# Performance work log

Hardware: AMD Instinct MI355X
Metric: run time of the kernel (lower is better)

The kernel has to match this reference:

```python
import jax, jax.numpy as jnp
import numpy as np

N, H, E, K = 256, 128, 64, 4  # nodes, hidden, dist-embed dim, heads
ALPHA = 0.2  # leaky-relu slope


def setup_inputs() -> dict:
    key = jax.random.key(0)
    ks = jax.random.split(key, 12)
    s = lambda k, sh: (jax.random.normal(k, sh, jnp.float32) * 0.05)
    return dict(
        action_hidden_state=jax.random.normal(ks[0], (N, H), jnp.float32),
        goal_hidden_state=jax.random.normal(ks[1], (N, H), jnp.float32),
        goal=jax.random.normal(ks[2], (N, 2), jnp.float32),
        action=jax.random.normal(ks[3], (N, 2), jnp.float32),
        W_emb=s(ks[4], (1, E)), b_emb=jnp.zeros((E,), jnp.float32),
        W_gate=s(ks[5], (2 * E + 2 * H, H)), b_gate=jnp.zeros((H,), jnp.float32),
        W_gat=s(ks[6], (K, H, H)), a_src=s(ks[7], (K, H)), a_dst=s(ks[8], (K, H)),
        gat_bias=jnp.zeros((H,), jnp.float32),
    )


def cal_dist(goal, action):
    # Vectorized, math-faithful (incl. source typos) version of the O(n^2) loop.
    ax, ay = action[:, 0], action[:, 1]
    gx, gy = goal[:, 0], goal[:, 1]
    a1x, a1y = ax[:, None], ay[:, None]   # node i
    a2x, a2y = ax[None, :], ay[None, :]   # node j
    g1x, g1y = gx[:, None], gy[:, None]
    g2x, g2y = gx[None, :], gy[None, :]
    dn = (a1x - a1x) * (g1y - g2y) - (a1y - a2y) * (g1x - g2x)
    cross_a = a1x * a2y - a1y * a2x
    gterm = g1x * g2y - g1x * g2x
    n1 = cross_a * (g1x - g2x) - (a1x - a2x) * gterm
    n2 = cross_a * (g1y - g2y) - (a1y - a2x) * gterm
    safe = jnp.where(dn == 0.0, 1.0, dn)
    p1, p2 = n1 / safe, n2 / safe
    base = jnp.linalg.norm(action - goal, axis=-1)  # [n]
    d1p = jnp.sqrt((a1x - p1) ** 2 + (a1y - p2) ** 2)
    d2p = jnp.sqrt((a2x - p1) ** 2 + (a2y - p2) ** 2)
    cond = (dn != 0.0) & ((a1x - p1) * (p1 - g1x) > 0.0)
    ones = jnp.ones_like(dn)
    d1 = jnp.where(cond, d1p, base[:, None] * ones)
    d2 = jnp.where(cond, d2p, base[None, :] * ones)
    n = d1.shape[0]
    ii = jnp.arange(n)[:, None]
    jj = jnp.arange(n)[None, :]
    # dist[i,j]=d1(i,j) for i<j; dist[j,i]=d2(i,j) i.e. lower triangle = d2.T; diag = |a_i - g_i|
    return jnp.where(ii == jj, base[:, None] * ones, jnp.where(ii < jj, d1, d2.T))


def reference(action_hidden_state, goal_hidden_state, goal, action,
              W_emb, b_emb, W_gate, b_gate, W_gat, a_src, a_dst, gat_bias):
    ha, hg = action_hidden_state, goal_hidden_state
    n, h = ha.shape
    dist = cal_dist(goal, action)                      # [n,n]
    emb = dist[..., None] * W_emb[0] + b_emb           # Linear(1,E) -> [n,n,E]
    # pairwise interaction gate (i != idx branch, computed for all pairs)
    gate_in = jnp.concatenate([
        jnp.broadcast_to(ha[:, None, :], (n, n, h)),
        jnp.broadcast_to(ha[None, :, :], (n, n, h)),
        emb, jnp.swapaxes(emb, 0, 1)], axis=-1)        # [n,n,2H+2E]
    gate = jax.nn.sigmoid(gate_in @ W_gate + b_gate)   # [n,n,H]
    gated = ha[None, :, :] * gate
    # self branch: gates the goal hidden state; action row stays ungated
    emb_d = emb[jnp.arange(n), jnp.arange(n)]          # [n,E]
    gate_self = jax.nn.sigmoid(
        jnp.concatenate([ha, hg, emb_d, emb_d], axis=-1) @ W_gate + b_gate)
    curr_goal = hg * gate_self                         # [n,H]
    eye = jnp.eye(n, dtype=bool)[..., None]
    curr_action = jnp.where(eye, ha[:, None, :], gated)          # [n,n,H]
    gat_in = jnp.concatenate([curr_action, curr_goal[:, None, :]], axis=1)  # [n,n+1,H]
    # multi-head GAT layer (batched over the n query nodes)
    hp = jnp.einsum('bmf,kfo->bkmo', gat_in, W_gat)    # [n,K,m,H]
    attn = (jnp.einsum('bkmo,ko->bkm', hp, a_src)[..., :, None]
            + jnp.einsum('bkmo,ko->bkm', hp, a_dst)[..., None, :])  # [n,K,m,m]
    attn = jax.nn.softmax(jax.nn.leaky_relu(attn, ALPHA), axis=-1)
    out = jnp.einsum('bkij,bkjo->bkio', attn, hp).mean(axis=1) + gat_bias  # [n,m,H]
    out = jax.nn.elu(out)
    idx = jnp.arange(n)
    return out[idx, idx]                               # [n,H]
```

## Files before the change

### kernel.cpp

```cpp
#include <hip/hip_runtime.h>
#include <math.h>

#define N 256
#define H 128
#define E 64
#define K 4
#define M (N + 1)
#define WAVES 16
#define BLOCK 1024

__device__ __forceinline__ float sigm(float x) {
    return __fdividef(1.0f, 1.0f + __expf(-x));
}

__device__ __forceinline__ float wave_sum(float v) {
#pragma unroll
    for (int d = 1; d < 64; d <<= 1) v += __shfl_xor(v, d, 64);
    return v;
}

__device__ __forceinline__ float readlane_f(float v, int l) {
    return __uint_as_float(__builtin_amdgcn_readlane(__float_as_uint(v), l));
}

__device__ __forceinline__ float kbutterfly(float q0, float q1, float q2, float q3,
                                            int lane) {
    const bool b1 = lane & 1;
    const bool b2 = lane & 2;
    float aA = b1 ? q1 : q0, aB = b1 ? q0 : q1;
    aA += __shfl_xor(aB, 1, 64);
    float cA = b1 ? q3 : q2, cB = b1 ? q2 : q3;
    cA += __shfl_xor(cB, 1, 64);
    float eA = b2 ? cA : aA, eB = b2 ? aA : cA;
    eA += __shfl_xor(eB, 2, 64);
#pragma unroll
    for (int d = 4; d < 64; d <<= 1) eA += __shfl_xor(eA, d, 64);
    return eA;
}

__device__ __forceinline__ void pairdist(
    float a1x, float a1y, float a2x, float a2y,
    float g1x, float g1y, float g2x, float g2y,
    float baseR, float baseC, float& d_rc, float& d_cr)
{
    float t  = __fmul_rn(__fsub_rn(a1y, a2y), __fsub_rn(g1x, g2x));
    float dn = -t;
    float ca = __fsub_rn(__fmul_rn(a1x, a2y), __fmul_rn(a1y, a2x));
    float gt = __fsub_rn(__fmul_rn(g1x, g2y), __fmul_rn(g1x, g2x));
    float n1 = __fsub_rn(__fmul_rn(ca, __fsub_rn(g1x, g2x)),
                         __fmul_rn(__fsub_rn(a1x, a2x), gt));
    float n2 = __fsub_rn(__fmul_rn(ca, __fsub_rn(g1y, g2y)),
                         __fmul_rn(__fsub_rn(a1y, a2x), gt));
    float safe = (dn == 0.0f) ? 1.0f : dn;
    float p1 = __fdiv_rn(n1, safe);
    float p2 = __fdiv_rn(n2, safe);
    bool cond = (dn != 0.0f) &&
                (__fmul_rn(__fsub_rn(a1x, p1), __fsub_rn(p1, g1x)) > 0.0f);
    float dx1 = __fsub_rn(a1x, p1), dy1 = __fsub_rn(a1y, p2);
    float d1p = __fsqrt_rn(__fadd_rn(__fmul_rn(dx1, dx1), __fmul_rn(dy1, dy1)));
    float dx2 = __fsub_rn(a2x, p1), dy2 = __fsub_rn(a2y, p2);
    float d2p = __fsqrt_rn(__fadd_rn(__fmul_rn(dx2, dx2), __fmul_rn(dy2, dy2)));
    d_rc = cond ? d1p : baseR;
    d_cr = cond ? d2p : baseC;
}

__global__ __launch_bounds__(BLOCK) void gat_pre(
    const float* __restrict__ ha, const float* __restrict__ hg,
    const float* __restrict__ W_emb, const float* __restrict__ b_emb,
    const float* __restrict__ W_gate, const float* __restrict__ b_gate,
    const float* __restrict__ W_gat, const float* __restrict__ a_src,
    const float* __restrict__ a_dst,
    float* __restrict__ A1, float* __restrict__ A2, float* __restrict__ G2,
    float* __restrict__ u3g, float* __restrict__ u4g, float* __restrict__ ccg,
    float* __restrict__ vsrc, float* __restrict__ vdst)
{
    const int b    = blockIdx.x;
    const int tid  = threadIdx.x;
    const int wid  = tid >> 6;
    const int lane = tid & 63;

    __shared__ float sRed[8][3][H];

    {
        const int f  = tid & (H - 1);
        const int sl = tid >> 7;
        const int g0 = sl * 16;
        float s1 = 0.f, s2 = 0.f, s3 = 0.f;
#pragma unroll
        for (int g = 0; g < 16; ++g) {
            const int gg = g0 + g;
            float w1 = W_gate[gg * H + f];
            float w2 = W_gate[(H + gg) * H + f];
            float av = ha[b * H + gg];
            float gv = hg[b * H + gg];
            s1 += av * w1;
            s2 += av * w2;
            s3 += gv * w2;
        }
        sRed[sl][0][f] = s1;
        sRed[sl][1][f] = s2;
        sRed[sl][2][f] = s3;
    }
    __syncthreads();
    if (tid < H) {
        float r1 = 0.f, r2 = 0.f, r3 = 0.f;
#pragma unroll
        for (int sl = 0; sl < 8; ++sl) {
            r1 += sRed[sl][0][tid];
            r2 += sRed[sl][1][tid];
            r3 += sRed[sl][2][tid];
        }
        A1[b * H + tid] = r1;
        A2[b * H + tid] = r2;
        G2[b * H + tid] = r3;
    }

    if (b < 8) {
        const int k = b >> 1;
        const float2 as = *(const float2*)&a_src[k * H + lane * 2];
        const float2 ad = *(const float2*)&a_dst[k * H + lane * 2];
#pragma unroll
        for (int it = 0; it < 4; ++it) {
            const int pair = b * 64 + wid * 4 + it;
            const int f    = pair & (H - 1);
            const float2 w = *(const float2*)&W_gat[(k * H + f) * H + lane * 2];
            float vs = wave_sum(w.x * as.x + w.y * as.y);
            float vv = wave_sum(w.x * ad.x + w.y * ad.y);
            if (lane == 0) { vsrc[k * H + f] = vs; vdst[k * H + f] = vv; }
        }
    } else if (b == 8) {
        __syncthreads();
        const int f  = tid & (H - 1);
        const int sl = tid >> 7;
        float s3 = 0.f, s4 = 0.f, scc = 0.f;
#pragma unroll
        for (int e0 = 0; e0 < 8; ++e0) {
            const int e = sl * 8 + e0;
            float w3 = W_gate[(2 * H + e) * H + f];
            float w4 = W_gate[(2 * H + E + e) * H + f];
            float we = W_emb[e], be = b_emb[e];
            s3  += we * w3;
            s4  += we * w4;
            scc += be * (w3 + w4);
        }
        sRed[sl][0][f] = s3;
        sRed[sl][1][f] = s4;
        sRed[sl][2][f] = scc;
        __syncthreads();
        if (tid < H) {
            float r3 = 0.f, r4 = 0.f, rc = 0.f;
#pragma unroll
            for (int sl = 0; sl < 8; ++sl) {
                r3 += sRed[sl][0][tid];
                r4 += sRed[sl][1][tid];
                rc += sRed[sl][2][tid];
            }
            u3g[tid] = r3;
            u4g[tid] = r4;
            ccg[tid] = rc + b_gate[tid];
        }
    }
}

__global__ __launch_bounds__(BLOCK) void gat_main(
    const float* __restrict__ ha, const float* __restrict__ hg,
    const float* __restrict__ W_gat, const float* __restrict__ gat_bias,
    const float* __restrict__ A1, const float* __restrict__ A2,
    const float* __restrict__ G2,
    const float* __restrict__ u3a, const float* __restrict__ u4a,
    const float* __restrict__ cca,
    const float* __restrict__ vsrc, const float* __restrict__ vdst,
    const float* __restrict__ goal, const float* __restrict__ action,
    float* __restrict__ out)
{
    const int i    = blockIdx.x;
    const int tid  = threadIdx.x;
    const int wid  = tid >> 6;
    const int lane = tid & 63;
    const int f0   = lane * 2;

    __shared__ float2 sAct[N];
    __shared__ float2 sGoal[N];
    __shared__ float  sBase[N];
    __shared__ float  sDij[M];
    __shared__ float  sDji[M];
    __shared__ float  sW[WAVES][K][H];
    __shared__ float  sMx[WAVES];
    __shared__ float  sL[WAVES][K];
    __shared__ float  sWfin[K][H];
    __shared__ float  sPart[8][H];

    const float2 a1v = *(const float2*)&A1[i * H + f0];
    const float2 haI = *(const float2*)&ha[i * H + f0];
    const float2 hgI = *(const float2*)&hg[i * H + f0];
    const float2 g2v = *(const float2*)&G2[i * H + f0];
    const float2 u3  = *(const float2*)&u3a[f0];
    const float2 u4  = *(const float2*)&u4a[f0];
    const float2 cc  = *(const float2*)&cca[f0];
    float2 vd0 = *(const float2*)&vdst[0 * H + f0];
    float2 vd1 = *(const float2*)&vdst[1 * H + f0];
    float2 vd2 = *(const float2*)&vdst[2 * H + f0];
    float2 vd3 = *(const float2*)&vdst[3 * H + f0];
    float2 vs0 = *(const float2*)&vsrc[0 * H + f0];
    float2 vs1 = *(const float2*)&vsrc[1 * H + f0];
    float2 vs2 = *(const float2*)&vsrc[2 * H + f0];
    float2 vs3 = *(const float2*)&vsrc[3 * H + f0];

    for (int t = tid; t < N; t += BLOCK) {
        float2 a = ((const float2*)action)[t];
        float2 g = ((const float2*)goal)[t];
        sAct[t]  = a;
        sGoal[t] = g;
        float dx = __fsub_rn(a.x, g.x), dy = __fsub_rn(a.y, g.y);
        sBase[t] = __fsqrt_rn(__fadd_rn(__fmul_rn(dx, dx), __fmul_rn(dy, dy)));
    }
    __syncthreads();

    if (tid < M) {
        const int j = tid;
        float dij = 0.f, dji = 0.f;
        if (j != i && j != N) {
            const float2 aI = sAct[i], gI = sGoal[i];
            const float2 aJ = sAct[j], gJ = sGoal[j];
            if (i < j)
                pairdist(aI.x, aI.y, aJ.x, aJ.y, gI.x, gI.y, gJ.x, gJ.y,
                         sBase[i], sBase[j], dij, dji);
            else
                pairdist(aJ.x, aJ.y, aI.x, aI.y, gJ.x, gJ.y, gI.x, gI.y,
                         sBase[j], sBase[i], dji, dij);
        }
        sDij[j] = dij;
        sDji[j] = dji;
    }

    const float scOwn = kbutterfly(haI.x * vs0.x + haI.y * vs0.y,
                                   haI.x * vs1.x + haI.y * vs1.y,
                                   haI.x * vs2.x + haI.y * vs2.y,
                                   haI.x * vs3.x + haI.y * vs3.y, lane);

    const float2 a1cc = make_float2(a1v.x + cc.x, a1v.y + cc.y);
    const float baseI = sBase[i];
    __syncthreads();

    float m_ = -INFINITY, l_ = 0.f;
    float w00 = 0.f, w01 = 0.f, w02 = 0.f, w03 = 0.f;
    float w10 = 0.f, w11 = 0.f, w12 = 0.f, w13 = 0.f;

    for (int g = 0; g < 4; ++g) {
        const int j0 = wid + 64 * g;

        float2 a2q[4], hhq[4];
        float dijq[4], djiq[4];
#pragma unroll
        for (int q = 0; q < 4; ++q) {
            const int j = j0 + 16 * q;
            a2q[q]  = *(const float2*)&A2[j * H + f0];
            hhq[q]  = *(const float2*)&ha[j * H + f0];
            dijq[q] = sDij[j];
            djiq[q] = sDji[j];
        }

        float2 gin[4];
#pragma unroll
        for (int q = 0; q < 4; ++q) {
            const int j = j0 + 16 * q;
            float tx = a1cc.x + a2q[q].x + dijq[q] * u3.x + djiq[q] * u4.x;
            float ty = a1cc.y + a2q[q].y + dijq[q] * u3.y + djiq[q] * u4.y;
            float2 gv = make_float2(hhq[q].x * sigm(tx), hhq[q].y * sigm(ty));
            gin[q] = (j == i) ? haI : gv;
        }

        float e[4];
#pragma unroll
        for (int q = 0; q < 4; ++q) {
            e[q] = kbutterfly(gin[q].x * vd0.x + gin[q].y * vd0.y,
                              gin[q].x * vd1.x + gin[q].y * vd1.y,
                              gin[q].x * vd2.x + gin[q].y * vd2.y,
                              gin[q].x * vd3.x + gin[q].y * vd3.y, lane);
        }

        float lg[4];
#pragma unroll
        for (int q = 0; q < 4; ++q) {
            float t = scOwn + e[q];
            lg[q] = (t >= 0.f) ? t : 0.2f * t;
        }

        float mm = fmaxf(fmaxf(lg[0], lg[1]), fmaxf(lg[2], lg[3]));
        mm = fmaxf(mm, __shfl_xor(mm, 1, 64));
        mm = fmaxf(mm, __shfl_xor(mm, 2, 64));
        if (mm > m_) {
            const float s = __expf(m_ - mm);
            l_ *= s;
            w00 *= s; w01 *= s; w02 *= s; w03 *= s;
            w10 *= s; w11 *= s; w12 *= s; w13 *= s;
            m_ = mm;
        }
        float p[4];
#pragma unroll
        for (int q = 0; q < 4; ++q) p[q] = __expf(lg[q] - m_);
        l_ += (p[0] + p[1]) + (p[2] + p[3]);

#pragma unroll
        for (int q = 0; q < 4; ++q) {
            const float p0 = readlane_f(p[q], 0), p1 = readlane_f(p[q], 1);
            const float p2 = readlane_f(p[q], 2), p3 = readlane_f(p[q], 3);
            w00 += p0 * gin[q].x;  w10 += p0 * gin[q].y;
            w01 += p1 * gin[q].x;  w11 += p1 * gin[q].y;
            w02 += p2 * gin[q].x;  w12 += p2 * gin[q].y;
            w03 += p3 * gin[q].x;  w13 += p3 * gin[q].y;
        }
    }

    if (wid == 0) {
        float tx = a1cc.x + g2v.x + baseI * (u3.x + u4.x);
        float ty = a1cc.y + g2v.y + baseI * (u3.y + u4.y);
        float2 gin = make_float2(hgI.x * sigm(tx), hgI.y * sigm(ty));

        float e = kbutterfly(gin.x * vd0.x + gin.y * vd0.y,
                             gin.x * vd1.x + gin.y * vd1.y,
                             gin.x * vd2.x + gin.y * vd2.y,
                             gin.x * vd3.x + gin.y * vd3.y, lane);
        float t  = scOwn + e;
        float lg = (t >= 0.f) ? t : 0.2f * t;
        float mm = fmaxf(lg, __shfl_xor(lg, 1, 64));
        mm = fmaxf(mm, __shfl_xor(mm, 2, 64));
        if (mm > m_) {
            const float s = __expf(m_ - mm);
            l_ *= s;
            w00 *= s; w01 *= s; w02 *= s; w03 *= s;
            w10 *= s; w11 *= s; w12 *= s; w13 *= s;
            m_ = mm;
        }
        const float p = __expf(lg - m_);
        l_ += p;
        const float p0 = readlane_f(p, 0), p1 = readlane_f(p, 1);
        const float p2 = readlane_f(p, 2), p3 = readlane_f(p, 3);
        w00 += p0 * gin.x;  w10 += p0 * gin.y;
        w01 += p1 * gin.x;  w11 += p1 * gin.y;
        w02 += p2 * gin.x;  w12 += p2 * gin.y;
        w03 += p3 * gin.x;  w13 += p3 * gin.y;
    }

    *(float2*)&sW[wid][0][f0] = make_float2(w00, w10);
    *(float2*)&sW[wid][1][f0] = make_float2(w01, w11);
    *(float2*)&sW[wid][2][f0] = make_float2(w02, w12);
    *(float2*)&sW[wid][3][f0] = make_float2(w03, w13);
    if (lane == 0) sMx[wid] = m_;
    if (lane < K)  sL[wid][lane] = l_;
    __syncthreads();

    if (tid < K * H) {
        const int k = tid >> 7;
        const int f = tid & (H - 1);
        float Mx = -INFINITY;
#pragma unroll
        for (int w = 0; w < WAVES; ++w) Mx = fmaxf(Mx, sMx[w]);
        float L = 0.f, W = 0.f;
#pragma unroll
        for (int w = 0; w < WAVES; ++w) {
            const float s = __expf(sMx[w] - Mx);
            L += s * sL[w][k];
            W += s * sW[w][k][f];
        }
        sWfin[k][f] = W / L;
    }
    __syncthreads();

    {
        const int f = tid & (H - 1);
        const int s = tid >> 7;
        float acc = 0.0f;
#pragma unroll
        for (int k = 0; k < K; ++k) {
            const int g0 = s * 16;
#pragma unroll
            for (int g = 0; g < 16; ++g)
                acc += sWfin[k][g0 + g] * W_gat[(k * H + g0 + g) * H + f];
        }
        sPart[s][f] = acc;
    }
    __syncthreads();

    if (tid < H) {
        float acc = 0.0f;
#pragma unroll
        for (int s = 0; s < 8; ++s) acc += sPart[s][tid];
        float val = 0.25f * acc + gat_bias[tid];
        out[i * H + tid] = (val > 0.0f) ? val : expm1f(val);
    }
}

extern "C" void kernel_launch(void* const* d_in, const int* in_sizes, int n_in,
                              void* d_out, int out_size, void* d_ws, size_t ws_size,
                              hipStream_t stream)
{
    const float* ha       = (const float*)d_in[0];
    const float* hg       = (const float*)d_in[1];
    const float* goal     = (const float*)d_in[2];
    const float* action   = (const float*)d_in[3];
    const float* W_emb    = (const float*)d_in[4];
    const float* b_emb    = (const float*)d_in[5];
    const float* W_gate   = (const float*)d_in[6];
    const float* b_gate   = (const float*)d_in[7];
    const float* W_gat    = (const float*)d_in[8];
    const float* a_src    = (const float*)d_in[9];
    const float* a_dst    = (const float*)d_in[10];
    const float* gat_bias = (const float*)d_in[11];

    float* ws  = (float*)d_ws;
    float* A1  = ws;
    float* A2  = A1 + N * H;
    float* G2  = A2 + N * H;
    float* u3  = G2 + N * H;
    float* u4  = u3 + H;
    float* cc  = u4 + H;
    float* vs  = cc + H;
    float* vd  = vs + K * H;

    hipLaunchKernelGGL(gat_pre, dim3(N), dim3(BLOCK), 0, stream,
                       ha, hg, W_emb, b_emb, W_gate, b_gate,
                       W_gat, a_src, a_dst,
                       A1, A2, G2, u3, u4, cc, vs, vd);

    hipLaunchKernelGGL(gat_main, dim3(N), dim3(BLOCK), 0, stream,
                       ha, hg, W_gat, gat_bias,
                       A1, A2, G2, u3, u4, cc, vs, vd,
                       goal, action, (float*)d_out);
}
```

Before: 29.54 us.

## Replace online softmax with two-pass block-wide softmax over shared logits

```diff
diff --git a/kernel.cpp b/kernel.cpp
--- a/kernel.cpp
+++ b/kernel.cpp
@@ -17,10 +17,6 @@
 #pragma unroll
     for (int d = 1; d < 64; d <<= 1) v += __shfl_xor(v, d, 64);
     return v;
-}
-
-__device__ __forceinline__ float readlane_f(float v, int l) {
-    return __uint_as_float(__builtin_amdgcn_readlane(__float_as_uint(v), l));
 }
 
 __device__ __forceinline__ float kbutterfly(float q0, float q1, float q2, float q3,
@@ -182,13 +178,17 @@
     __shared__ float2 sAct[N];
     __shared__ float2 sGoal[N];
     __shared__ float  sBase[N];
-    __shared__ float  sDij[M];
-    __shared__ float  sDji[M];
-    __shared__ float  sW[WAVES][K][H];
-    __shared__ float  sMx[WAVES];
-    __shared__ float  sL[WAVES][K];
+    __shared__ float2 sD[M];
+    __shared__ __align__(16) float pbuf[M * K + 4];
+    __shared__ float  ssc[K];
+    __shared__ float  sMred[WAVES];
+    __shared__ float  sLpart[WAVES];
+    __shared__ float  sLk[K];
     __shared__ float  sWfin[K][H];
-    __shared__ float  sPart[8][H];
+    __shared__ __align__(16) char uBuf[34048];
+    float* uPart = (float*)uBuf;
+    float (*uSW)[K][H]  = (float (*)[K][H])uBuf;
+    float (*uEp)[H]     = (float (*)[H])uBuf;
 
     const float2 a1v = *(const float2*)&A1[i * H + f0];
     const float2 haI = *(const float2*)&ha[i * H + f0];
@@ -197,14 +197,14 @@
     const float2 u3  = *(const float2*)&u3a[f0];
     const float2 u4  = *(const float2*)&u4a[f0];
     const float2 cc  = *(const float2*)&cca[f0];
-    float2 vd0 = *(const float2*)&vdst[0 * H + f0];
-    float2 vd1 = *(const float2*)&vdst[1 * H + f0];
-    float2 vd2 = *(const float2*)&vdst[2 * H + f0];
-    float2 vd3 = *(const float2*)&vdst[3 * H + f0];
-    float2 vs0 = *(const float2*)&vsrc[0 * H + f0];
-    float2 vs1 = *(const float2*)&vsrc[1 * H + f0];
-    float2 vs2 = *(const float2*)&vsrc[2 * H + f0];
-    float2 vs3 = *(const float2*)&vsrc[3 * H + f0];
+    const float2 vd0 = *(const float2*)&vdst[0 * H + f0];
+    const float2 vd1 = *(const float2*)&vdst[1 * H + f0];
+    const float2 vd2 = *(const float2*)&vdst[2 * H + f0];
+    const float2 vd3 = *(const float2*)&vdst[3 * H + f0];
+    const float2 vs0 = *(const float2*)&vsrc[0 * H + f0];
+    const float2 vs1 = *(const float2*)&vsrc[1 * H + f0];
+    const float2 vs2 = *(const float2*)&vsrc[2 * H + f0];
+    const float2 vs3 = *(const float2*)&vsrc[3 * H + f0];
 
     for (int t = tid; t < N; t += BLOCK) {
         float2 a = ((const float2*)action)[t];
@@ -229,141 +229,141 @@
                 pairdist(aJ.x, aJ.y, aI.x, aI.y, gJ.x, gJ.y, gI.x, gI.y,
                          sBase[j], sBase[i], dji, dij);
         }
-        sDij[j] = dij;
-        sDji[j] = dji;
+        sD[j] = make_float2(dij, dji);
     }
 
     const float scOwn = kbutterfly(haI.x * vs0.x + haI.y * vs0.y,
                                    haI.x * vs1.x + haI.y * vs1.y,
                                    haI.x * vs2.x + haI.y * vs2.y,
                                    haI.x * vs3.x + haI.y * vs3.y, lane);
+    if (wid == 0 && lane < K) ssc[lane] = scOwn;
 
     const float2 a1cc = make_float2(a1v.x + cc.x, a1v.y + cc.y);
     const float baseI = sBase[i];
     __syncthreads();
 
-    float m_ = -INFINITY, l_ = 0.f;
-    float w00 = 0.f, w01 = 0.f, w02 = 0.f, w03 = 0.f;
-    float w10 = 0.f, w11 = 0.f, w12 = 0.f, w13 = 0.f;
-
-    for (int g = 0; g < 4; ++g) {
-        const int j0 = wid + 64 * g;
-
-        float2 a2q[4], hhq[4];
-        float dijq[4], djiq[4];
-#pragma unroll
-        for (int q = 0; q < 4; ++q) {
-            const int j = j0 + 16 * q;
-            a2q[q]  = *(const float2*)&A2[j * H + f0];
-            hhq[q]  = *(const float2*)&ha[j * H + f0];
-            dijq[q] = sDij[j];
-            djiq[q] = sDji[j];
-        }
-
-        float2 gin[4];
-#pragma unroll
-        for (int q = 0; q < 4; ++q) {
-            const int j = j0 + 16 * q;
-            float tx = a1cc.x + a2q[q].x + dijq[q] * u3.x + djiq[q] * u4.x;
-            float ty = a1cc.y + a2q[q].y + dijq[q] * u3.y + djiq[q] * u4.y;
-            float2 gv = make_float2(hhq[q].x * sigm(tx), hhq[q].y * sigm(ty));
-            gin[q] = (j == i) ? haI : gv;
-        }
-
-        float e[4];
-#pragma unroll
-        for (int q = 0; q < 4; ++q) {
-            e[q] = kbutterfly(gin[q].x * vd0.x + gin[q].y * vd0.y,
-                              gin[q].x * vd1.x + gin[q].y * vd1.y,
-                              gin[q].x * vd2.x + gin[q].y * vd2.y,
-                              gin[q].x * vd3.x + gin[q].y * vd3.y, lane);
-        }
-
-        float lg[4];
-#pragma unroll
-        for (int q = 0; q < 4; ++q) {
-            float t = scOwn + e[q];
-            lg[q] = (t >= 0.f) ? t : 0.2f * t;
-        }
-
-        float mm = fmaxf(fmaxf(lg[0], lg[1]), fmaxf(lg[2], lg[3]));
-        mm = fmaxf(mm, __shfl_xor(mm, 1, 64));
-        mm = fmaxf(mm, __shfl_xor(mm, 2, 64));
-        if (mm > m_) {
-            const float s = __expf(m_ - mm);
-            l_ *= s;
-            w00 *= s; w01 *= s; w02 *= s; w03 *= s;
-            w10 *= s; w11 *= s; w12 *= s; w13 *= s;
-            m_ = mm;
-        }
-        float p[4];
-#pragma unroll
-        for (int q = 0; q < 4; ++q) p[q] = __expf(lg[q] - m_);
-        l_ += (p[0] + p[1]) + (p[2] + p[3]);
-
-#pragma unroll
-        for (int q = 0; q < 4; ++q) {
-            const float p0 = readlane_f(p[q], 0), p1 = readlane_f(p[q], 1);
-            const float p2 = readlane_f(p[q], 2), p3 = readlane_f(p[q], 3);
-            w00 += p0 * gin[q].x;  w10 += p0 * gin[q].y;
-            w01 += p1 * gin[q].x;  w11 += p1 * gin[q].y;
-            w02 += p2 * gin[q].x;  w12 += p2 * gin[q].y;
-            w03 += p3 * gin[q].x;  w13 += p3 * gin[q].y;
-        }
-    }
-
+    const bool b1 = lane & 1;
+    const bool b2 = lane & 2;
+    const int  wrIdx   = ((lane >> 3) << 2) + (lane & 3);
+    const bool doWrite = !(lane & 4);
+    float2 gin[16];
+
+#pragma unroll
+    for (int t = 0; t < 16; ++t) {
+        const int jj = wid + 16 * t;
+        const float2 a2 = *(const float2*)&A2[jj * H + f0];
+        const float2 hj = *(const float2*)&ha[jj * H + f0];
+        const float2 d  = sD[jj];
+        float tx = a1cc.x + a2.x + d.x * u3.x + d.y * u4.x;
+        float ty = a1cc.y + a2.y + d.x * u3.y + d.y * u4.y;
+        float2 g = make_float2(hj.x * sigm(tx), hj.y * sigm(ty));
+        if (jj == i) g = haI;
+        gin[t] = g;
+        float q0 = g.x * vd0.x + g.y * vd0.y;
+        float q1 = g.x * vd1.x + g.y * vd1.y;
+        float q2 = g.x * vd2.x + g.y * vd2.y;
+        float q3 = g.x * vd3.x + g.y * vd3.y;
+        float aA = b1 ? q1 : q0, aB = b1 ? q0 : q1;
+        aA += __shfl_xor(aB, 1, 64);
+        float cA = b1 ? q3 : q2, cB = b1 ? q2 : q3;
+        cA += __shfl_xor(cB, 1, 64);
+        float eA = b2 ? cA : aA, eB = b2 ? aA : cA;
+        eA += __shfl_xor(eB, 2, 64);
+        eA += __shfl_xor(eA, 4, 64);
+        if (doWrite) uPart[jj * 33 + wrIdx] = eA;
+    }
+
+    float2 ginG = make_float2(0.f, 0.f);
     if (wid == 0) {
         float tx = a1cc.x + g2v.x + baseI * (u3.x + u4.x);
         float ty = a1cc.y + g2v.y + baseI * (u3.y + u4.y);
-        float2 gin = make_float2(hgI.x * sigm(tx), hgI.y * sigm(ty));
-
-        float e = kbutterfly(gin.x * vd0.x + gin.y * vd0.y,
-                             gin.x * vd1.x + gin.y * vd1.y,
-                             gin.x * vd2.x + gin.y * vd2.y,
-                             gin.x * vd3.x + gin.y * vd3.y, lane);
-        float t  = scOwn + e;
-        float lg = (t >= 0.f) ? t : 0.2f * t;
-        float mm = fmaxf(lg, __shfl_xor(lg, 1, 64));
-        mm = fmaxf(mm, __shfl_xor(mm, 2, 64));
-        if (mm > m_) {
-            const float s = __expf(m_ - mm);
-            l_ *= s;
-            w00 *= s; w01 *= s; w02 *= s; w03 *= s;
-            w10 *= s; w11 *= s; w12 *= s; w13 *= s;
-            m_ = mm;
-        }
-        const float p = __expf(lg - m_);
-        l_ += p;
-        const float p0 = readlane_f(p, 0), p1 = readlane_f(p, 1);
-        const float p2 = readlane_f(p, 2), p3 = readlane_f(p, 3);
-        w00 += p0 * gin.x;  w10 += p0 * gin.y;
-        w01 += p1 * gin.x;  w11 += p1 * gin.y;
-        w02 += p2 * gin.x;  w12 += p2 * gin.y;
-        w03 += p3 * gin.x;  w13 += p3 * gin.y;
-    }
-
-    *(float2*)&sW[wid][0][f0] = make_float2(w00, w10);
-    *(float2*)&sW[wid][1][f0] = make_float2(w01, w11);
-    *(float2*)&sW[wid][2][f0] = make_float2(w02, w12);
-    *(float2*)&sW[wid][3][f0] = make_float2(w03, w13);
-    if (lane == 0) sMx[wid] = m_;
-    if (lane < K)  sL[wid][lane] = l_;
+        ginG = make_float2(hgI.x * sigm(tx), hgI.y * sigm(ty));
+        float q0 = ginG.x * vd0.x + ginG.y * vd0.y;
+        float q1 = ginG.x * vd1.x + ginG.y * vd1.y;
+        float q2 = ginG.x * vd2.x + ginG.y * vd2.y;
+        float q3 = ginG.x * vd3.x + ginG.y * vd3.y;
+        float aA = b1 ? q1 : q0, aB = b1 ? q0 : q1;
+        aA += __shfl_xor(aB, 1, 64);
+        float cA = b1 ? q3 : q2, cB = b1 ? q2 : q3;
+        cA += __shfl_xor(cB, 1, 64);
+        float eA = b2 ? cA : aA, eB = b2 ? aA : cA;
+        eA += __shfl_xor(eB, 2, 64);
+        eA += __shfl_xor(eA, 4, 64);
+        if (doWrite) uPart[N * 33 + wrIdx] = eA;
+    }
+    __syncthreads();
+
+    const int jq = tid & 255;
+    const int kq = tid >> 8;
+    float dd = 0.f;
+#pragma unroll
+    for (int g = 0; g < 8; ++g) dd += uPart[jq * 33 + g * 4 + kq];
+    float lgq = ssc[kq] + dd;
+    lgq = (lgq >= 0.f) ? lgq : 0.2f * lgq;
+
+    float lgT = -INFINITY;
+    if (tid < 4) {
+        float ddT = 0.f;
+#pragma unroll
+        for (int g = 0; g < 8; ++g) ddT += uPart[N * 33 + g * 4 + tid];
+        lgT = ssc[tid] + ddT;
+        lgT = (lgT >= 0.f) ? lgT : 0.2f * lgT;
+    }
+
+    float mx = fmaxf(lgq, lgT);
+#pragma unroll
+    for (int d = 1; d < 64; d <<= 1) mx = fmaxf(mx, __shfl_xor(mx, d, 64));
+    if (lane == 0) sMred[wid] = mx;
+    __syncthreads();
+
+    float Mg = sMred[0];
+#pragma unroll
+    for (int w = 1; w < WAVES; ++w) Mg = fmaxf(Mg, sMred[w]);
+
+    const float pq = __expf(lgq - Mg);
+    pbuf[jq * 4 + kq] = pq;
+    if (tid < 4) pbuf[N * 4 + tid] = __expf(lgT - Mg);
+
+    const float lp = wave_sum(pq);
+    if (lane == 0) sLpart[wid] = lp;
+    __syncthreads();
+    if (tid < 4)
+        sLk[tid] = sLpart[tid * 4 + 0] + sLpart[tid * 4 + 1] +
+                   sLpart[tid * 4 + 2] + sLpart[tid * 4 + 3] +
+                   pbuf[N * 4 + tid];
+
+    float w00 = 0.f, w01 = 0.f, w02 = 0.f, w03 = 0.f;
+    float w10 = 0.f, w11 = 0.f, w12 = 0.f, w13 = 0.f;
+#pragma unroll
+    for (int t = 0; t < 16; ++t) {
+        const int jj = wid + 16 * t;
+        const float4 p4 = *(const float4*)&pbuf[jj * 4];
+        w00 += p4.x * gin[t].x;  w10 += p4.x * gin[t].y;
+        w01 += p4.y * gin[t].x;  w11 += p4.y * gin[t].y;
+        w02 += p4.z * gin[t].x;  w12 += p4.z * gin[t].y;
+        w03 += p4.w * gin[t].x;  w13 += p4.w * gin[t].y;
+    }
+    if (wid == 0) {
+        const float4 p4 = *(const float4*)&pbuf[N * 4];
+        w00 += p4.x * ginG.x;  w10 += p4.x * ginG.y;
+        w01 += p4.y * ginG.x;  w11 += p4.y * ginG.y;
+        w02 += p4.z * ginG.x;  w12 += p4.z * ginG.y;
+        w03 += p4.w * ginG.x;  w13 += p4.w * ginG.y;
+    }
+
+    *(float2*)&uSW[wid][0][f0] = make_float2(w00, w10);
+    *(float2*)&uSW[wid][1][f0] = make_float2(w01, w11);
+    *(float2*)&uSW[wid][2][f0] = make_float2(w02, w12);
+    *(float2*)&uSW[wid][3][f0] = make_float2(w03, w13);
     __syncthreads();
 
     if (tid < K * H) {
         const int k = tid >> 7;
         const int f = tid & (H - 1);
-        float Mx = -INFINITY;
-#pragma unroll
-        for (int w = 0; w < WAVES; ++w) Mx = fmaxf(Mx, sMx[w]);
-        float L = 0.f, W = 0.f;
-#pragma unroll
-        for (int w = 0; w < WAVES; ++w) {
-            const float s = __expf(sMx[w] - Mx);
-            L += s * sL[w][k];
-            W += s * sW[w][k][f];
-        }
-        sWfin[k][f] = W / L;
+        float W = 0.f;
+#pragma unroll
+        for (int w = 0; w < WAVES; ++w) W += uSW[w][k][f];
+        sWfin[k][f] = W / sLk[k];
     }
     __syncthreads();
 
@@ -378,14 +378,15 @@
             for (int g = 0; g < 16; ++g)
                 acc += sWfin[k][g0 + g] * W_gat[(k * H + g0 + g) * H + f];
         }
-        sPart[s][f] = acc;
+        __syncthreads();
+        uEp[s][f] = acc;
     }
     __syncthreads();
 
     if (tid < H) {
         float acc = 0.0f;
 #pragma unroll
-        for (int s = 0; s < 8; ++s) acc += sPart[s][tid];
+        for (int s = 0; s < 8; ++s) acc += uEp[s][tid];
         float val = 0.25f * acc + gat_bias[tid];
         out[i * H + tid] = (val > 0.0f) ? val : expm1f(val);
     }
```

New measurement: 28.05 us. 1.05x faster.
